# Performance work log

Measured on AMD Instinct MI355X. Metric: run time of the kernel, lower is better.

The kernel has to match this reference:

```python
import jax, jax.numpy as jnp
import numpy as np

# --- Mamba2 dims (TP=1) ---
D_MODEL = 2048
D_STATE = 128
D_CONV = 4
NHEADS = 64
NGROUPS = 8
HEAD_DIM = 64
CHUNK = 256
SEQLEN = 2048
EPS = 1e-5
D_INNER = NHEADS * HEAD_DIM                      # 4096
CONV_DIM = D_INNER + 2 * NGROUPS * D_STATE        # 6144
D_IN_PROJ = 2 * D_INNER + 2 * NGROUPS * D_STATE + NHEADS  # 10304
HPG = NHEADS // NGROUPS                           # heads per group = 8


def _silu(x):
    return x * jax.nn.sigmoid(x)


def setup_inputs() -> dict:
    key = jax.random.key(0)
    ks = jax.random.split(key, 9)
    n = lambda k, shape, s: jax.random.normal(k, shape, jnp.float32) * s
    A = -jnp.exp(jax.random.uniform(ks[4], (NHEADS,), jnp.float32,
                                    np.log(1.0), np.log(16.0)))  # negative, Mamba2-style
    return {
        "hidden_states": n(ks[0], (SEQLEN, D_MODEL), 1.0),
        "in_proj_w": n(ks[1], (D_IN_PROJ, D_MODEL), 0.02),
        "conv_w": n(ks[2], (CONV_DIM, D_CONV), 0.2),
        "conv_b": n(ks[3], (CONV_DIM,), 0.02),
        "A": A,
        "D_param": n(ks[5], (NHEADS,), 1.0),
        "dt_bias": n(ks[6], (NHEADS,), 0.5),
        "norm_w": jnp.ones((D_INNER,), jnp.float32),
        "out_proj_w": n(ks[8], (D_MODEL, D_INNER), 0.02),
    }


def reference(hidden_states, in_proj_w, conv_w, conv_b, A, D_param, dt_bias, norm_w, out_proj_w):
    T = hidden_states.shape[0]
    # in_proj: packed [z | xbc | dt]
    zxbcdt = hidden_states @ in_proj_w.T                          # [T, D_IN_PROJ]
    z = zxbcdt[:, :D_INNER]                                       # gate
    xbc = zxbcdt[:, D_INNER:D_INNER + CONV_DIM]
    dt_raw = zxbcdt[:, D_INNER + CONV_DIM:]                       # [T, H]

    # causal depthwise conv1d + SiLU (K=4, small fixed unroll)
    xpad = jnp.pad(xbc, ((D_CONV - 1, 0), (0, 0)))
    win = jnp.stack([xpad[i:i + T] for i in range(D_CONV)], axis=-1)  # [T, C, K]
    xbc = _silu(jnp.einsum('tck,ck->tc', win, conv_w) + conv_b)

    x = xbc[:, :D_INNER]
    Bm = xbc[:, D_INNER:D_INNER + NGROUPS * D_STATE]
    Cm = xbc[:, D_INNER + NGROUPS * D_STATE:]

    nc = T // CHUNK
    # heads are laid out contiguously per group: H = (G, HPG)
    x = x.reshape(nc, CHUNK, NGROUPS, HPG, HEAD_DIM)              # [c,l,g,r,p]
    Bm = Bm.reshape(nc, CHUNK, NGROUPS, D_STATE)                  # [c,l,g,n]
    Cm = Cm.reshape(nc, CHUNK, NGROUPS, D_STATE)
    dt = jax.nn.softplus(dt_raw + dt_bias).reshape(nc, CHUNK, NGROUPS, HPG)  # [c,l,g,r]

    Ag = A.reshape(NGROUPS, HPG)
    dA = dt * Ag                                                  # [c,l,g,r]
    dA_cs = jnp.cumsum(dA, axis=1)                                # cumulative within chunk

    # --- intra-chunk (quadratic within chunk) ---
    CB = jnp.einsum('csgn,ctgn->cgst', Cm, Bm)                    # [c,g,s,t]
    dA_t = jnp.transpose(dA_cs, (0, 2, 3, 1))                     # [c,g,r,l]
    diff = dA_t[..., :, None] - dA_t[..., None, :]                # [c,g,r,s,t]
    causal = jnp.tril(jnp.ones((CHUNK, CHUNK), bool))
    decay = jnp.where(causal, jnp.exp(diff), 0.0)
    dt_t = jnp.transpose(dt, (0, 2, 3, 1))                        # [c,g,r,t]
    scores = CB[:, :, None] * decay * dt_t[..., None, :]          # [c,g,r,s,t]
    y = jnp.einsum('cgrst,ctgrp->csgrp', scores, x)

    # --- per-chunk end states ---
    decay_last = jnp.exp(dA_cs[:, -1:, :, :] - dA_cs)             # [c,l,g,r]
    states = jnp.einsum('ctgn,ctgr,ctgrp->cgrpn', Bm, decay_last * dt, x)

    # --- inter-chunk recurrence (scan over chunks) ---
    chunk_decay = jnp.exp(dA_cs[:, -1])                           # [c,g,r]
    def step(carry, inp):
        st, dec = inp
        return carry * dec[..., None, None] + st, carry
    _, prev = jax.lax.scan(step, jnp.zeros_like(states[0]), (states, chunk_decay))
    # prev[c] = state entering chunk c, shape [c,g,r,p,n]

    y = y + jnp.einsum('csgn,csgr,cgrpn->csgrp', Cm, jnp.exp(dA_cs), prev)
    y = y + D_param.reshape(NGROUPS, HPG)[None, None, :, :, None] * x

    y = y.reshape(T, D_INNER)
    # gated grouped RMSNorm (norm_before_gate=False, group_size = D_INNER // NGROUPS)
    y = y * _silu(z)
    yg = y.reshape(T, NGROUPS, D_INNER // NGROUPS)
    var = jnp.mean(yg * yg, axis=-1, keepdims=True)
    y = (yg * jax.lax.rsqrt(var + EPS)).reshape(T, D_INNER) * norm_w

    return y @ out_proj_w.T                                       # [T, D_MODEL]
```

## Files before the change

### kernel.cpp

```cpp
#include <hip/hip_runtime.h>
#include <math.h>

#define T_SEQ 2048
#define DMODEL 2048
#define DSTATE 128
#define NH 64
#define NG 8
#define HPG 8
#define HD 64
#define CH 256
#define NC 8
#define DIN 4096
#define CONVD 6144
#define DPROJ 10304
#define DPROJP 10368
#define BCW 2048
#define DTOFF 10240
#define EPS 1e-5f

typedef short v8s __attribute__((ext_vector_type(8)));
typedef float v4f __attribute__((ext_vector_type(4)));

__device__ __forceinline__ float silu_f(float x) { return x / (1.0f + __expf(-x)); }

__device__ __forceinline__ unsigned short f2b(float x) {
    union { float f; unsigned u; } v; v.f = x;
    unsigned r = v.u + 0x7fffu + ((v.u >> 16) & 1u);
    return (unsigned short)(r >> 16);
}
__device__ __forceinline__ float b2f(unsigned short u) {
    union { unsigned u; float f; } v; v.u = ((unsigned)u) << 16; return v.f;
}

__global__ __launch_bounds__(256) void cvt_front(const float4* __restrict__ wsrc,
                                                 ushort4* __restrict__ wdst,
                                                 int n4s_w, int n4d_w,
                                                 const float4* __restrict__ hsrc,
                                                 ushort4* __restrict__ hdst, int n4_h) {
    int i = blockIdx.x * 256 + threadIdx.x;
    if (i < n4d_w) {
        ushort4 o = {0, 0, 0, 0};
        if (i < n4s_w) {
            float4 v = wsrc[i];
            o.x = f2b(v.x); o.y = f2b(v.y); o.z = f2b(v.z); o.w = f2b(v.w);
        }
        wdst[i] = o;
    } else {
        int j = i - n4d_w;
        if (j < n4_h) {
            float4 v = hsrc[j];
            ushort4 o = {f2b(v.x), f2b(v.y), f2b(v.z), f2b(v.w)};
            hdst[j] = o;
        }
    }
}

template <int BN, bool OUTB>
__global__ __launch_bounds__(256) void gemm_bf16(const unsigned short* __restrict__ A,
                                                 const unsigned short* __restrict__ B,
                                                 float* __restrict__ Cf,
                                                 unsigned short* __restrict__ Cbo,
                                                 float* __restrict__ dtout,
                                                 int M, int N, int K, int nbase) {
    constexpr int BM = 128, BK = 32;
    constexpr int NWT = BN / 32;
    constexpr int BCH = (BN * BK * 2) / 1024;
    __shared__ short sA[BM * BK];
    __shared__ short sB[BN * BK];
    const int tid = threadIdx.x;
    const int wave = tid >> 6, lane = tid & 63;
    const int m0 = blockIdx.x * BM, n0 = blockIdx.y * BN;
    const int wm = (wave >> 1) * 64;
    const int wn = (wave & 1) * (BN / 2);
    const int lr = lane & 15, kq = lane >> 4;

    v4f acc[4][NWT];
#pragma unroll
    for (int i = 0; i < 4; ++i)
#pragma unroll
        for (int j = 0; j < NWT; ++j) acc[i][j] = {0.f, 0.f, 0.f, 0.f};

    for (int k0 = 0; k0 < K; k0 += BK) {
#pragma unroll
        for (int qi = 0; qi < 2; ++qi) {
            int q = wave * 2 + qi;
            int e = q * 512 + lane * 8;
            int r = e >> 5, c = e & 31;
            __builtin_amdgcn_global_load_lds(
                (const __attribute__((address_space(1))) void*)(A + (size_t)(m0 + r) * K + k0 + c),
                (__attribute__((address_space(3))) void*)(sA + q * 512), 16, 0, 0);
        }
        for (int q = wave; q < BCH; q += 4) {
            int e = q * 512 + lane * 8;
            int r = e >> 5, c = e & 31;
            __builtin_amdgcn_global_load_lds(
                (const __attribute__((address_space(1))) void*)(B + (size_t)(n0 + r) * K + k0 + c),
                (__attribute__((address_space(3))) void*)(sB + q * 512), 16, 0, 0);
        }
        __syncthreads();
        v8s af[4], bf[NWT];
#pragma unroll
        for (int i = 0; i < 4; ++i)
            af[i] = *(const v8s*)(sA + (wm + i * 16 + lr) * BK + kq * 8);
#pragma unroll
        for (int j = 0; j < NWT; ++j)
            bf[j] = *(const v8s*)(sB + (wn + j * 16 + lr) * BK + kq * 8);
#pragma unroll
        for (int i = 0; i < 4; ++i)
#pragma unroll
            for (int j = 0; j < NWT; ++j)
                acc[i][j] = __builtin_amdgcn_mfma_f32_16x16x32_bf16(af[i], bf[j], acc[i][j], 0, 0, 0);
        __syncthreads();
    }
    const int crow = kq * 4, ccol = lr;
#pragma unroll
    for (int i = 0; i < 4; ++i)
#pragma unroll
        for (int j = 0; j < NWT; ++j) {
            const int col = nbase + n0 + wn + j * 16 + ccol;
            const int row0 = m0 + wm + i * 16 + crow;
#pragma unroll
            for (int r = 0; r < 4; ++r) {
                float v = acc[i][j][r];
                if (OUTB) {
                    Cbo[(size_t)(row0 + r) * N + col] = f2b(v);
                    if ((unsigned)(col - DTOFF) < 64u)
                        dtout[(size_t)(row0 + r) * 64 + (col - DTOFF)] = v;
                } else {
                    Cf[(size_t)(row0 + r) * N + col] = v;
                }
            }
        }
}

template <int BN, bool OUTB>
__global__ __launch_bounds__(256) void gemm64_bf16(const unsigned short* __restrict__ A,
                                                   const unsigned short* __restrict__ B,
                                                   float* __restrict__ Cf,
                                                   unsigned short* __restrict__ Cbo,
                                                   float* __restrict__ dtout,
                                                   int M, int N, int K, int nbase) {
    constexpr int BM = 128, BK = 64;
    constexpr int NWT = BN / 32;
    constexpr int BSEGW = BN / 32;
    __shared__ short sA[BM * BK];
    __shared__ short sB[BN * BK];
    const int tid = threadIdx.x;
    const int wave = tid >> 6, lane = tid & 63;
    const int m0 = blockIdx.x * BM, n0 = blockIdx.y * BN;
    const int wm = (wave >> 1) * 64;
    const int wn = (wave & 1) * (BN / 2);
    const int lr = lane & 15, kq = lane >> 4;

    const int r8 = lane >> 3, c8 = lane & 7;
    const int gq = (c8 ^ r8) * 8;
    const int ck0 = ((kq) ^ (lr & 7)) * 8;
    const int ck1 = ((kq + 4) ^ (lr & 7)) * 8;

    v4f acc[4][NWT];
#pragma unroll
    for (int i = 0; i < 4; ++i)
#pragma unroll
        for (int j = 0; j < NWT; ++j) acc[i][j] = {0.f, 0.f, 0.f, 0.f};

    for (int k0 = 0; k0 < K; k0 += BK) {
#pragma unroll
        for (int s = 0; s < 4; ++s) {
            const int seg = wave * 4 + s;
            const int r = seg * 8 + r8;
            __builtin_amdgcn_global_load_lds(
                (const __attribute__((address_space(1))) void*)(A + (size_t)(m0 + r) * K + k0 + gq),
                (__attribute__((address_space(3))) void*)(sA + seg * 512 + lane * 8), 16, 0, 0);
        }
#pragma unroll
        for (int s = 0; s < BSEGW; ++s) {
            const int seg = wave * BSEGW + s;
            const int r = seg * 8 + r8;
            __builtin_amdgcn_global_load_lds(
                (const __attribute__((address_space(1))) void*)(B + (size_t)(n0 + r) * K + k0 + gq),
                (__attribute__((address_space(3))) void*)(sB + seg * 512 + lane * 8), 16, 0, 0);
        }
        __syncthreads();
#pragma unroll
        for (int kk = 0; kk < 2; ++kk) {
            const int ck = kk ? ck1 : ck0;
            v8s af[4], bf[NWT];
#pragma unroll
            for (int i = 0; i < 4; ++i)
                af[i] = *(const v8s*)(sA + (wm + i * 16 + lr) * BK + ck);
#pragma unroll
            for (int j = 0; j < NWT; ++j)
                bf[j] = *(const v8s*)(sB + (wn + j * 16 + lr) * BK + ck);
#pragma unroll
            for (int i = 0; i < 4; ++i)
#pragma unroll
                for (int j = 0; j < NWT; ++j)
                    acc[i][j] = __builtin_amdgcn_mfma_f32_16x16x32_bf16(af[i], bf[j], acc[i][j], 0, 0, 0);
        }
        __syncthreads();
    }
    const int crow = kq * 4, ccol = lr;
#pragma unroll
    for (int i = 0; i < 4; ++i)
#pragma unroll
        for (int j = 0; j < NWT; ++j) {
            const int col = nbase + n0 + wn + j * 16 + ccol;
            const int row0 = m0 + wm + i * 16 + crow;
#pragma unroll
            for (int r = 0; r < 4; ++r) {
                float v = acc[i][j][r];
                if (OUTB) {
                    Cbo[(size_t)(row0 + r) * N + col] = f2b(v);
                    if ((unsigned)(col - DTOFF) < 64u)
                        dtout[(size_t)(row0 + r) * 64 + (col - DTOFF)] = v;
                } else {
                    Cf[(size_t)(row0 + r) * N + col] = v;
                }
            }
        }
}

__global__ __launch_bounds__(256) void convdt_kernel(const unsigned short* __restrict__ zxb,
                                                     const float* __restrict__ cw,
                                                     const float* __restrict__ cb,
                                                     unsigned short* __restrict__ Xt,
                                                     unsigned short* __restrict__ BCb,
                                                     unsigned short* __restrict__ Btr,
                                                     const float* __restrict__ dt_raw,
                                                     const float* __restrict__ A,
                                                     const float* __restrict__ dt_bias,
                                                     float* __restrict__ dt_s,
                                                     float* __restrict__ dAcs) {
    __shared__ unsigned short sh[64 * 262];
    const int tid = threadIdx.x;
    if (blockIdx.x < NC * 96) {
        const int cc = blockIdx.x / 96, cg = blockIdx.x % 96;
        const int c0 = cg * 64;
        const int cl = tid & 63, tq = tid >> 6;
        const int ch = c0 + cl;
        const float4 w = ((const float4*)cw)[ch];
        const float bias = cb[ch];
        const int tg0 = cc * 256 + tq * 64;
        float x0 = (tg0 >= 3) ? b2f(zxb[(size_t)(tg0 - 3) * DPROJP + DIN + ch]) : 0.f;
        float x1 = (tg0 >= 2) ? b2f(zxb[(size_t)(tg0 - 2) * DPROJP + DIN + ch]) : 0.f;
        float x2 = (tg0 >= 1) ? b2f(zxb[(size_t)(tg0 - 1) * DPROJP + DIN + ch]) : 0.f;
#pragma unroll 8
        for (int i = 0; i < 64; ++i) {
            float x3 = b2f(zxb[(size_t)(tg0 + i) * DPROJP + DIN + ch]);
            float acc = bias + x0 * w.x + x1 * w.y + x2 * w.z + x3 * w.w;
            sh[cl * 262 + tq * 64 + i] = f2b(silu_f(acc));
            x0 = x1; x1 = x2; x2 = x3;
        }
        __syncthreads();
        if (c0 < DIN) {
            const int h = c0 >> 6;
            unsigned short* dst = Xt + (size_t)(cc * NH + h) * HD * CH;
#pragma unroll
            for (int it = 0; it < 8; ++it) {
                int flat = it * 256 + tid;
                int row = flat >> 5, col = (flat & 31) * 8;
                *(ushort4*)&dst[(size_t)row * CH + col]     = *(ushort4*)&sh[row * 262 + col];
                *(ushort4*)&dst[(size_t)row * CH + col + 4] = *(ushort4*)&sh[row * 262 + col + 4];
            }
        } else {
            const int bc0 = c0 - DIN;
            for (int it = 0; it < 64; ++it) {
                int t = it * 4 + tq;
                BCb[(size_t)(cc * 256 + t) * BCW + bc0 + cl] = sh[cl * 262 + t];
            }
            if (bc0 < NG * DSTATE) {
                unsigned short* dst = Btr + ((size_t)cc * (NG * DSTATE) + bc0) * CH;
#pragma unroll
                for (int it = 0; it < 8; ++it) {
                    int flat = it * 256 + tid;
                    int row = flat >> 5, col = (flat & 31) * 8;
                    *(ushort4*)&dst[(size_t)row * CH + col]     = *(ushort4*)&sh[row * 262 + col];
                    *(ushort4*)&dst[(size_t)row * CH + col + 4] = *(ushort4*)&sh[row * 262 + col + 4];
                }
            }
        }
    } else {
        float* s = (float*)sh;
        const int bid = blockIdx.x - NC * 96;
        int h = bid % NH, c = bid / NH;
        int t = tid;
        int tg = c * CH + t;
        float raw = dt_raw[(size_t)tg * 64 + h] + dt_bias[h];
        float dtv = (raw > 20.0f) ? raw : log1pf(__expf(raw));
        s[t] = dtv * A[h];
        __syncthreads();
        for (int off = 1; off < CH; off <<= 1) {
            float add = (t >= off) ? s[t - off] : 0.0f;
            __syncthreads();
            s[t] += add;
            __syncthreads();
        }
        dt_s[h * T_SEQ + tg] = dtv;
        dAcs[h * T_SEQ + tg] = s[t];
    }
}

__global__ __launch_bounds__(256) void states_mfma(const unsigned short* __restrict__ Xt,
                                                   const unsigned short* __restrict__ Btr,
                                                   const float* __restrict__ dt_s,
                                                   const float* __restrict__ dAcs,
                                                   float* __restrict__ states) {
    __shared__ float w2sh[CH];
    const int h = blockIdx.x % NH, c = blockIdx.x / NH, g = h >> 3;
    const int tid = threadIdx.x, wave = tid >> 6, lane = tid & 63;
    const int lr = lane & 15, quad = lane >> 4;
    float da_last = dAcs[h * T_SEQ + c * CH + CH - 1];
    w2sh[tid] = __expf(da_last - dAcs[h * T_SEQ + c * CH + tid]) * dt_s[h * T_SEQ + c * CH + tid];
    __syncthreads();
    const unsigned short* Xr = Xt + (size_t)(c * NH + h) * HD * CH;
    const unsigned short* Br = Btr + (size_t)(c * NG + g) * DSTATE * CH;

    v4f acc[4][2];
#pragma unroll
    for (int i = 0; i < 4; ++i)
#pragma unroll
        for (int j = 0; j < 2; ++j) acc[i][j] = {0.f, 0.f, 0.f, 0.f};

    for (int kb = 0; kb < 8; ++kb) {
        const int t0 = kb * 32 + quad * 8;
        float w[8];
        {
            float4 wa = *(const float4*)&w2sh[t0];
            float4 wb = *(const float4*)&w2sh[t0 + 4];
            w[0] = wa.x; w[1] = wa.y; w[2] = wa.z; w[3] = wa.w;
            w[4] = wb.x; w[5] = wb.y; w[6] = wb.z; w[7] = wb.w;
        }
        v8s bf[2];
#pragma unroll
        for (int j = 0; j < 2; ++j) {
            v8s raw = *(const v8s*)(Br + (size_t)(wave * 32 + j * 16 + lr) * CH + t0);
            v8s o;
#pragma unroll
            for (int e = 0; e < 8; ++e) o[e] = (short)f2b(b2f((unsigned short)raw[e]) * w[e]);
            bf[j] = o;
        }
        v8s af[4];
#pragma unroll
        for (int i = 0; i < 4; ++i)
            af[i] = *(const v8s*)(Xr + (size_t)(i * 16 + lr) * CH + t0);
#pragma unroll
        for (int i = 0; i < 4; ++i)
#pragma unroll
            for (int j = 0; j < 2; ++j)
                acc[i][j] = __builtin_amdgcn_mfma_f32_16x16x32_bf16(af[i], bf[j], acc[i][j], 0, 0, 0);
    }
#pragma unroll
    for (int i = 0; i < 4; ++i)
#pragma unroll
        for (int j = 0; j < 2; ++j)
#pragma unroll
            for (int r = 0; r < 4; ++r)
                states[((size_t)(c * NH + h) * HD + i * 16 + quad * 4 + r) * DSTATE +
                       wave * 32 + j * 16 + lr] = acc[i][j][r];
}

__global__ __launch_bounds__(256) void scan_kernel(const float* __restrict__ states,
                                                   const float* __restrict__ dAcs,
                                                   unsigned short* __restrict__ prev_b) {
    int h = blockIdx.x >> 3, seg = blockIdx.x & 7;
    int base = seg * 1024 + threadIdx.x * 4;
    float4 carry = {0.f, 0.f, 0.f, 0.f};
    for (int c = 0; c < NC; ++c) {
        size_t off = (size_t)(c * NH + h) * (HD * DSTATE) + base;
        ushort4 o = {f2b(carry.x), f2b(carry.y), f2b(carry.z), f2b(carry.w)};
        *(ushort4*)&prev_b[off] = o;
        float cd = __expf(dAcs[h * T_SEQ + c * CH + CH - 1]);
        float4 s = *(const float4*)&states[off];
        carry.x = fmaf(carry.x, cd, s.x);
        carry.y = fmaf(carry.y, cd, s.y);
        carry.z = fmaf(carry.z, cd, s.z);
        carry.w = fmaf(carry.w, cd, s.w);
    }
}

__global__ __launch_bounds__(256) void y12_mfma(const unsigned short* __restrict__ BCb,
                                                const unsigned short* __restrict__ Xt,
                                                const unsigned short* __restrict__ prev_b,
                                                const float* __restrict__ dt_s,
                                                const float* __restrict__ dAcs,
                                                const float* __restrict__ Dp,
                                                float* __restrict__ yacc) {
    __shared__ float s_da[CH], s_dt[CH];
    __shared__ unsigned short pw[4][16][40];
    const int h = blockIdx.x % NH, c = blockIdx.x / NH, g = h >> 3;
    const int tid = threadIdx.x, wave = tid >> 6, lane = tid & 63;
    const int lr = lane & 15, quad = lane >> 4;
    s_da[tid] = dAcs[h * T_SEQ + c * CH + tid];
    s_dt[tid] = dt_s[h * T_SEQ + c * CH + tid];
    __syncthreads();

    const unsigned short* Cb = BCb + (size_t)c * CH * BCW + NG * DSTATE + g * DSTATE;
    const unsigned short* Bb = BCb + (size_t)c * CH * BCW + g * DSTATE;
    const unsigned short* Xr = Xt + (size_t)(c * NH + h) * HD * CH;
    const unsigned short* Pr = prev_b + (size_t)(c * NH + h) * HD * DSTATE;
    const float Dh = Dp[h];

    v4f Y[4][4];
#pragma unroll
    for (int i = 0; i < 4; ++i)
#pragma unroll
        for (int j = 0; j < 4; ++j) Y[i][j] = {0.f, 0.f, 0.f, 0.f};

    {
        float es[4];
#pragma unroll
        for (int i = 0; i < 4; ++i) es[i] = __expf(s_da[(i * 4 + wave) * 16 + lr]);
#pragma unroll
        for (int kb = 0; kb < 4; ++kb) {
            const int n0 = kb * 32 + quad * 8;
            v8s bfp[4];
#pragma unroll
            for (int pj = 0; pj < 4; ++pj)
                bfp[pj] = *(const v8s*)(Pr + (size_t)(pj * 16 + lr) * DSTATE + n0);
#pragma unroll
            for (int i = 0; i < 4; ++i) {
                int st = i * 4 + wave;
                v8s raw = *(const v8s*)(Cb + (size_t)(st * 16 + lr) * BCW + n0);
                v8s af;
#pragma unroll
                for (int e = 0; e < 8; ++e) af[e] = (short)f2b(b2f((unsigned short)raw[e]) * es[i]);
#pragma unroll
                for (int pj = 0; pj < 4; ++pj)
                    Y[i][pj] = __builtin_amdgcn_mfma_f32_16x16x32_bf16(af, bfp[pj], Y[i][pj], 0, 0, 0);
            }
        }
    }

    for (int tb = 0; tb < 8; ++tb) {
        if (12 + wave < 2 * tb) continue;
        const int t0q = tb * 32 + quad * 8;
        v8s xf[4];
#pragma unroll
        for (int pj = 0; pj < 4; ++pj)
            xf[pj] = *(const v8s*)(Xr + (size_t)(pj * 16 + lr) * CH + t0q);
        v8s bfr[2][4];
#pragma unroll
        for (int j = 0; j < 2; ++j)
#pragma unroll
            for (int ks = 0; ks < 4; ++ks)
                bfr[j][ks] = *(const v8s*)(Bb + (size_t)(tb * 32 + j * 16 + lr) * BCW + ks * 32 + quad * 8);
#pragma unroll
        for (int i = 0; i < 4; ++i) {
            int st = i * 4 + wave;
            if (st < 2 * tb) continue;
            v4f S0 = {0.f, 0.f, 0.f, 0.f}, S1 = {0.f, 0.f, 0.f, 0.f};
#pragma unroll
            for (int ks = 0; ks < 4; ++ks) {
                v8s af = *(const v8s*)(Cb + (size_t)(st * 16 + lr) * BCW + ks * 32 + quad * 8);
                S0 = __builtin_amdgcn_mfma_f32_16x16x32_bf16(af, bfr[0][ks], S0, 0, 0, 0);
                S1 = __builtin_amdgcn_mfma_f32_16x16x32_bf16(af, bfr[1][ks], S1, 0, 0, 0);
            }
            int t0 = tb * 32 + lr;
            float da0 = s_da[t0], dt0 = s_dt[t0];
            float da1 = s_da[t0 + 16], dt1 = s_dt[t0 + 16];
#pragma unroll
            for (int r = 0; r < 4; ++r) {
                int s = st * 16 + quad * 4 + r;
                float das = s_da[s];
                float w0 = (t0 <= s) ? S0[r] * __expf(das - da0) * dt0 : 0.f;
                float w1 = (t0 + 16 <= s) ? S1[r] * __expf(das - da1) * dt1 : 0.f;
                if (t0 == s) w0 += Dh;
                if (t0 + 16 == s) w1 += Dh;
                pw[wave][quad * 4 + r][lr] = f2b(w0);
                pw[wave][quad * 4 + r][16 + lr] = f2b(w1);
            }
            v8s pf = *(const v8s*)(&pw[wave][lr][quad * 8]);
#pragma unroll
            for (int pj = 0; pj < 4; ++pj)
                Y[i][pj] = __builtin_amdgcn_mfma_f32_16x16x32_bf16(pf, xf[pj], Y[i][pj], 0, 0, 0);
        }
    }
#pragma unroll
    for (int i = 0; i < 4; ++i) {
        int st = i * 4 + wave;
#pragma unroll
        for (int pj = 0; pj < 4; ++pj) {
            int p = pj * 16 + lr;
#pragma unroll
            for (int r = 0; r < 4; ++r) {
                int s = st * 16 + quad * 4 + r;
                yacc[(size_t)(c * CH + s) * DIN + h * HD + p] = Y[i][pj][r];
            }
        }
    }
}

__global__ __launch_bounds__(256) void normcvt_kernel(const unsigned short* __restrict__ zxb,
                                                      const float* __restrict__ yacc,
                                                      const float* __restrict__ norm_w,
                                                      unsigned short* __restrict__ ynorm,
                                                      const float4* __restrict__ osrc,
                                                      ushort4* __restrict__ odst) {
    if (blockIdx.x < 8192) {
        __shared__ float red[4];
        const int sub = threadIdx.x >> 7, tid = threadIdx.x & 127;
        const int gid = blockIdx.x * 2 + sub;
        const int t = gid / NG, g = gid % NG;
        const int j = g * 512 + tid * 4;
        float4 y4 = *(const float4*)&yacc[(size_t)t * DIN + j];
        ushort4 z4 = *(const ushort4*)&zxb[(size_t)t * DPROJP + j];
        float v0 = y4.x * silu_f(b2f(z4.x));
        float v1 = y4.y * silu_f(b2f(z4.y));
        float v2 = y4.z * silu_f(b2f(z4.z));
        float v3 = y4.w * silu_f(b2f(z4.w));
        float ss = v0 * v0 + v1 * v1 + v2 * v2 + v3 * v3;
#pragma unroll
        for (int off = 32; off > 0; off >>= 1) ss += __shfl_down(ss, off, 64);
        if ((threadIdx.x & 63) == 0) red[threadIdx.x >> 6] = ss;
        __syncthreads();
        float var = (red[sub * 2] + red[sub * 2 + 1]) * (1.0f / 512.0f);
        float scale = rsqrtf(var + EPS);
        float4 w4 = *(const float4*)&norm_w[j];
        ushort4 o = {f2b(v0 * scale * w4.x), f2b(v1 * scale * w4.y),
                     f2b(v2 * scale * w4.z), f2b(v3 * scale * w4.w)};
        *(ushort4*)&ynorm[(size_t)t * DIN + j] = o;
    } else {
        int i = (blockIdx.x - 8192) * 256 + threadIdx.x;
        float4 v = osrc[i];
        ushort4 o = {f2b(v.x), f2b(v.y), f2b(v.z), f2b(v.w)};
        odst[i] = o;
    }
}

extern "C" void kernel_launch(void* const* d_in, const int* in_sizes, int n_in,
                              void* d_out, int out_size, void* d_ws, size_t ws_size,
                              hipStream_t stream) {
    const float* hidden     = (const float*)d_in[0];
    const float* in_proj_w  = (const float*)d_in[1];
    const float* conv_w     = (const float*)d_in[2];
    const float* conv_b     = (const float*)d_in[3];
    const float* A          = (const float*)d_in[4];
    const float* Dp         = (const float*)d_in[5];
    const float* dt_bias    = (const float*)d_in[6];
    const float* norm_w     = (const float*)d_in[7];
    const float* out_proj_w = (const float*)d_in[8];
    float* out = (float*)d_out;

    float* ws     = (float*)d_ws;
    unsigned short* zxb = (unsigned short*)ws;
    float* dt_raw = ws + 10616832;
    float* dt_s   = dt_raw + 131072;
    float* dAcs   = dt_s + 131072;
    float* yacc   = dAcs + 131072;
    float* regE   = yacc + 8388608;
    float* regF   = regE + 10616832;

    unsigned short* inw_b  = (unsigned short*)regE;
    unsigned short* Xt_b   = (unsigned short*)regE;
    float*          states = regE + 4194304;
    unsigned short* outw_b = (unsigned short*)regE;
    unsigned short* hidden_b = (unsigned short*)regF;
    unsigned short* BCb      = (unsigned short*)regF;
    unsigned short* Btr      = (unsigned short*)(regF + 2097152);
    unsigned short* prev_b   = (unsigned short*)(regF + 2097152);
    unsigned short* ynorm_b  = (unsigned short*)regF;

    {
        int n4s = DPROJ * DMODEL / 4, n4d = DPROJP * DMODEL / 4;
        int h4 = T_SEQ * DMODEL / 4;
        cvt_front<<<(n4d + h4 + 255) / 256, 256, 0, stream>>>(
            (const float4*)in_proj_w, (ushort4*)inw_b, n4s, n4d,
            (const float4*)hidden, (ushort4*)hidden_b, h4);
    }
    gemm_bf16<128, true><<<dim3(T_SEQ / 128, DPROJP / 128), 256, 0, stream>>>(
        hidden_b, inw_b, nullptr, zxb, dt_raw, T_SEQ, DPROJP, DMODEL, 0);

    convdt_kernel<<<NC * 96 + NC * NH, 256, 0, stream>>>(
        zxb, conv_w, conv_b, Xt_b, BCb, Btr, dt_raw, A, dt_bias, dt_s, dAcs);

    states_mfma<<<NC * NH, 256, 0, stream>>>(Xt_b, Btr, dt_s, dAcs, states);
    scan_kernel<<<NH * 8, 256, 0, stream>>>(states, dAcs, prev_b);
    y12_mfma<<<NC * NH, 256, 0, stream>>>(BCb, Xt_b, prev_b, dt_s, dAcs, Dp, yacc);

    normcvt_kernel<<<16384, 256, 0, stream>>>(
        zxb, yacc, norm_w, ynorm_b, (const float4*)out_proj_w, (ushort4*)outw_b);

    gemm64_bf16<64, false><<<dim3(T_SEQ / 128, DMODEL / 64), 256, 0, stream>>>(
        ynorm_b, outw_b, out, nullptr, nullptr, T_SEQ, DMODEL, DIN, 0);
}
```

Baseline: 449.1 us.

## Remap GEMM tiles across XCDs, raise MFMA priority, defer C decay scaling

Both GEMMs now launch a 1D grid and remap block IDs so consecutive tiles on each of the 8 XCDs share A rows, which should improve L2 reuse on the chiplet layout. s_setprio brackets around MFMA loops in the states and y kernels favor matrix issue over other waves. In the inter-chunk y term, the per-row exp(dA_cs) scaling moves from a bf16 rescale of C before the MFMA to an fp32 multiply on the accumulator afterwards. This drops per-element conversions and also slightly changes rounding. The remap relies on the grid size being divisible by 8 (16*81 and 16*32 both are).

```diff
diff --git a/kernel.cpp b/kernel.cpp
--- a/kernel.cpp
+++ b/kernel.cpp
@@ -61,7 +61,7 @@
                                                  float* __restrict__ Cf,
                                                  unsigned short* __restrict__ Cbo,
                                                  float* __restrict__ dtout,
-                                                 int M, int N, int K, int nbase) {
+                                                 int M, int N, int K, int nbase, int mt) {
     constexpr int BM = 128, BK = 32;
     constexpr int NWT = BN / 32;
     constexpr int BCH = (BN * BK * 2) / 1024;
@@ -69,7 +69,9 @@
     __shared__ short sB[BN * BK];
     const int tid = threadIdx.x;
     const int wave = tid >> 6, lane = tid & 63;
-    const int m0 = blockIdx.x * BM, n0 = blockIdx.y * BN;
+    const int q = (int)gridDim.x >> 3;
+    const int wg = ((int)blockIdx.x & 7) * q + ((int)blockIdx.x >> 3);
+    const int m0 = (wg % mt) * BM, n0 = (wg / mt) * BN;
     const int wm = (wave >> 1) * 64;
     const int wn = (wave & 1) * (BN / 2);
     const int lr = lane & 15, kq = lane >> 4;
@@ -83,19 +85,19 @@
     for (int k0 = 0; k0 < K; k0 += BK) {
 #pragma unroll
         for (int qi = 0; qi < 2; ++qi) {
-            int q = wave * 2 + qi;
-            int e = q * 512 + lane * 8;
+            int qq = wave * 2 + qi;
+            int e = qq * 512 + lane * 8;
             int r = e >> 5, c = e & 31;
             __builtin_amdgcn_global_load_lds(
                 (const __attribute__((address_space(1))) void*)(A + (size_t)(m0 + r) * K + k0 + c),
-                (__attribute__((address_space(3))) void*)(sA + q * 512), 16, 0, 0);
-        }
-        for (int q = wave; q < BCH; q += 4) {
-            int e = q * 512 + lane * 8;
+                (__attribute__((address_space(3))) void*)(sA + qq * 512), 16, 0, 0);
+        }
+        for (int qq = wave; qq < BCH; qq += 4) {
+            int e = qq * 512 + lane * 8;
             int r = e >> 5, c = e & 31;
             __builtin_amdgcn_global_load_lds(
                 (const __attribute__((address_space(1))) void*)(B + (size_t)(n0 + r) * K + k0 + c),
-                (__attribute__((address_space(3))) void*)(sB + q * 512), 16, 0, 0);
+                (__attribute__((address_space(3))) void*)(sB + qq * 512), 16, 0, 0);
         }
         __syncthreads();
         v8s af[4], bf[NWT];
@@ -139,7 +141,7 @@
                                                    float* __restrict__ Cf,
                                                    unsigned short* __restrict__ Cbo,
                                                    float* __restrict__ dtout,
-                                                   int M, int N, int K, int nbase) {
+                                                   int M, int N, int K, int nbase, int mt) {
     constexpr int BM = 128, BK = 64;
     constexpr int NWT = BN / 32;
     constexpr int BSEGW = BN / 32;
@@ -147,7 +149,9 @@
     __shared__ short sB[BN * BK];
     const int tid = threadIdx.x;
     const int wave = tid >> 6, lane = tid & 63;
-    const int m0 = blockIdx.x * BM, n0 = blockIdx.y * BN;
+    const int q = (int)gridDim.x >> 3;
+    const int wg = ((int)blockIdx.x & 7) * q + ((int)blockIdx.x >> 3);
+    const int m0 = (wg % mt) * BM, n0 = (wg / mt) * BN;
     const int wm = (wave >> 1) * 64;
     const int wn = (wave & 1) * (BN / 2);
     const int lr = lane & 15, kq = lane >> 4;
@@ -343,11 +347,13 @@
 #pragma unroll
         for (int i = 0; i < 4; ++i)
             af[i] = *(const v8s*)(Xr + (size_t)(i * 16 + lr) * CH + t0);
+        __builtin_amdgcn_s_setprio(1);
 #pragma unroll
         for (int i = 0; i < 4; ++i)
 #pragma unroll
             for (int j = 0; j < 2; ++j)
                 acc[i][j] = __builtin_amdgcn_mfma_f32_16x16x32_bf16(af[i], bf[j], acc[i][j], 0, 0, 0);
+        __builtin_amdgcn_s_setprio(0);
     }
 #pragma unroll
     for (int i = 0; i < 4; ++i)
@@ -406,28 +412,32 @@
 #pragma unroll
         for (int j = 0; j < 4; ++j) Y[i][j] = {0.f, 0.f, 0.f, 0.f};
 
-    {
-        float es[4];
-#pragma unroll
-        for (int i = 0; i < 4; ++i) es[i] = __expf(s_da[(i * 4 + wave) * 16 + lr]);
-#pragma unroll
-        for (int kb = 0; kb < 4; ++kb) {
-            const int n0 = kb * 32 + quad * 8;
-            v8s bfp[4];
+#pragma unroll
+    for (int kb = 0; kb < 4; ++kb) {
+        const int n0 = kb * 32 + quad * 8;
+        v8s bfp[4];
+#pragma unroll
+        for (int pj = 0; pj < 4; ++pj)
+            bfp[pj] = *(const v8s*)(Pr + (size_t)(pj * 16 + lr) * DSTATE + n0);
+        __builtin_amdgcn_s_setprio(1);
+#pragma unroll
+        for (int i = 0; i < 4; ++i) {
+            int st = i * 4 + wave;
+            v8s af = *(const v8s*)(Cb + (size_t)(st * 16 + lr) * BCW + n0);
 #pragma unroll
             for (int pj = 0; pj < 4; ++pj)
-                bfp[pj] = *(const v8s*)(Pr + (size_t)(pj * 16 + lr) * DSTATE + n0);
-#pragma unroll
-            for (int i = 0; i < 4; ++i) {
-                int st = i * 4 + wave;
-                v8s raw = *(const v8s*)(Cb + (size_t)(st * 16 + lr) * BCW + n0);
-                v8s af;
-#pragma unroll
-                for (int e = 0; e < 8; ++e) af[e] = (short)f2b(b2f((unsigned short)raw[e]) * es[i]);
-#pragma unroll
-                for (int pj = 0; pj < 4; ++pj)
-                    Y[i][pj] = __builtin_amdgcn_mfma_f32_16x16x32_bf16(af, bfp[pj], Y[i][pj], 0, 0, 0);
-            }
+                Y[i][pj] = __builtin_amdgcn_mfma_f32_16x16x32_bf16(af, bfp[pj], Y[i][pj], 0, 0, 0);
+        }
+        __builtin_amdgcn_s_setprio(0);
+    }
+#pragma unroll
+    for (int i = 0; i < 4; ++i) {
+        int st = i * 4 + wave;
+#pragma unroll
+        for (int r = 0; r < 4; ++r) {
+            float es = __expf(s_da[st * 16 + quad * 4 + r]);
+#pragma unroll
+            for (int pj = 0; pj < 4; ++pj) Y[i][pj][r] *= es;
         }
     }
 
@@ -449,12 +459,14 @@
             int st = i * 4 + wave;
             if (st < 2 * tb) continue;
             v4f S0 = {0.f, 0.f, 0.f, 0.f}, S1 = {0.f, 0.f, 0.f, 0.f};
+            __builtin_amdgcn_s_setprio(1);
 #pragma unroll
             for (int ks = 0; ks < 4; ++ks) {
                 v8s af = *(const v8s*)(Cb + (size_t)(st * 16 + lr) * BCW + ks * 32 + quad * 8);
                 S0 = __builtin_amdgcn_mfma_f32_16x16x32_bf16(af, bfr[0][ks], S0, 0, 0, 0);
                 S1 = __builtin_amdgcn_mfma_f32_16x16x32_bf16(af, bfr[1][ks], S1, 0, 0, 0);
             }
+            __builtin_amdgcn_s_setprio(0);
             int t0 = tb * 32 + lr;
             float da0 = s_da[t0], dt0 = s_dt[t0];
             float da1 = s_da[t0 + 16], dt1 = s_dt[t0 + 16];
@@ -470,9 +482,11 @@
                 pw[wave][quad * 4 + r][16 + lr] = f2b(w1);
             }
             v8s pf = *(const v8s*)(&pw[wave][lr][quad * 8]);
+            __builtin_amdgcn_s_setprio(1);
 #pragma unroll
             for (int pj = 0; pj < 4; ++pj)
                 Y[i][pj] = __builtin_amdgcn_mfma_f32_16x16x32_bf16(pf, xf[pj], Y[i][pj], 0, 0, 0);
+            __builtin_amdgcn_s_setprio(0);
         }
     }
 #pragma unroll
@@ -567,8 +581,8 @@
             (const float4*)in_proj_w, (ushort4*)inw_b, n4s, n4d,
             (const float4*)hidden, (ushort4*)hidden_b, h4);
     }
-    gemm_bf16<128, true><<<dim3(T_SEQ / 128, DPROJP / 128), 256, 0, stream>>>(
-        hidden_b, inw_b, nullptr, zxb, dt_raw, T_SEQ, DPROJP, DMODEL, 0);
+    gemm_bf16<128, true><<<dim3(16 * 81), 256, 0, stream>>>(
+        hidden_b, inw_b, nullptr, zxb, dt_raw, T_SEQ, DPROJP, DMODEL, 0, 16);
 
     convdt_kernel<<<NC * 96 + NC * NH, 256, 0, stream>>>(
         zxb, conv_w, conv_b, Xt_b, BCb, Btr, dt_raw, A, dt_bias, dt_s, dAcs);
@@ -580,6 +594,6 @@
     normcvt_kernel<<<16384, 256, 0, stream>>>(
         zxb, yacc, norm_w, ynorm_b, (const float4*)out_proj_w, (ushort4*)outw_b);
 
-    gemm64_bf16<64, false><<<dim3(T_SEQ / 128, DMODEL / 64), 256, 0, stream>>>(
-        ynorm_b, outw_b, out, nullptr, nullptr, T_SEQ, DMODEL, DIN, 0);
-}
+    gemm64_bf16<64, false><<<dim3(16 * 32), 256, 0, stream>>>(
+        ynorm_b, outw_b, out, nullptr, nullptr, T_SEQ, DMODEL, DIN, 0, 16);
+}
```

Result: no change. 452.5 us (+0.8%).
